# Performance work log

Hardware: AMD Instinct MI355X
Metric: run time of the kernel (lower is better)

## Reference

```python
import jax, jax.numpy as jnp
import numpy as np

D = 6          # stalk dimension
F = 64         # MLP_hidden / feature dim
N = 100_000    # num nodes
E = 20_000     # num hyperedges
NNZ = 1_000_000  # incidences
LN_EPS = 1e-5


def setup_inputs() -> dict:
    key = jax.random.key(0)
    ks = jax.random.split(key, 6)
    x = jax.random.normal(ks[0], (N * D, F), dtype=jnp.float32)
    e = jax.random.normal(ks[1], (E * D, F), dtype=jnp.float32)
    row = jax.random.randint(ks[2], (NNZ,), 0, N)   # node index per incidence
    col = jax.random.randint(ks[3], (NNZ,), 0, E)   # hyperedge index per incidence
    ln_gamma = jnp.ones((2 * F,), jnp.float32)
    ln_beta = jnp.zeros((2 * F,), jnp.float32)
    W = jax.random.normal(ks[4], (2 * F, D), dtype=jnp.float32) / np.sqrt(2 * F)
    b = jnp.zeros((D,), jnp.float32)
    return dict(x=x, e=e, row=row, col=col, ln_gamma=ln_gamma, ln_beta=ln_beta, W=W, b=b)


def reference(x, e, row, col, ln_gamma, ln_beta, W, b):
    # collapse stalk dim: [N*d, F] -> [N, F]
    n = x.shape[0] // D
    m = e.shape[0] // D
    xm = x.reshape(n, D, -1).mean(axis=1)
    em = e.reshape(m, D, -1).mean(axis=1)
    # var1 hyperedge features: gather per incidence
    xs = xm[row]            # [nnz, F]
    es = em[col]            # [nnz, F]
    h = jnp.concatenate([xs, es], axis=-1)  # [nnz, 2F]
    # sheaf_lin = input LayerNorm + Linear (num_layers=1 MLP)
    mu = h.mean(axis=-1, keepdims=True)
    var = h.var(axis=-1, keepdims=True)
    h = (h - mu) * jax.lax.rsqrt(var + LN_EPS) * ln_gamma + ln_beta
    h = h @ W + b           # [nnz, D]
    return jax.nn.sigmoid(h)  # sheaf_act='sigmoid'
```

## Files before the change

### kernel.cpp

```cpp
#include <hip/hip_runtime.h>

#define DD 6
#define FF 64
#define LN_EPS 1e-5f

template <int CTRL>
__device__ inline float dpp_mov(float x) {
    return __int_as_float(__builtin_amdgcn_update_dpp(
        0, __float_as_int(x), CTRL, 0xF, 0xF, true));
}

__global__ __launch_bounds__(256) void entity_kernel(
    const float* __restrict__ x, const float* __restrict__ e,
    const float* __restrict__ gamma, const float* __restrict__ beta,
    const float* __restrict__ W, const float* __restrict__ b,
    float* __restrict__ nodeT, float* __restrict__ edgeT,
    float* __restrict__ gwbw, int N, int E) {
    if (blockIdx.x == 0 && threadIdx.x < 12) {
        const int t = threadIdx.x;
        const int j = (t < 6) ? t : t - 6;
        const float* g = (t < 6) ? gamma : beta;
        float s = (t < 6) ? 0.f : b[j];
        for (int k = 0; k < 2 * FF; ++k) s = fmaf(g[k], W[k * DD + j], s);
        gwbw[t] = s;
    }

    const int gl = threadIdx.x & 15;
    const int nodePairs = (N + 1) >> 1;
    const int edgePairs = (E + 1) >> 1;
    const int p = blockIdx.x * 16 + (threadIdx.x >> 4);
    if (p >= nodePairs + edgePairs) return;

    const float* in; float* tab; int A, last, kbase;
    if (p < nodePairs) {
        in = x; tab = nodeT; A = 2 * p; last = N - 1; kbase = 0;
    } else {
        in = e; tab = edgeT; A = 2 * (p - nodePairs); last = E - 1; kbase = FF;
    }
    const int B = A + 1;
    const bool bval = (B <= last);
    const int Bc = bval ? B : A;

    const float4* pa = reinterpret_cast<const float4*>(in + (size_t)A * (DD * FF)) + gl;
    const float4* pb = reinterpret_cast<const float4*>(in + (size_t)Bc * (DD * FF)) + gl;
    float4 va[DD], vb[DD];
#pragma unroll
    for (int d = 0; d < DD; ++d) { va[d] = pa[d * 16]; vb[d] = pb[d * 16]; }

    float gwl[4][6];
#pragma unroll
    for (int c = 0; c < 4; ++c) {
        const int k = kbase + 4 * gl + c;
        const float g = gamma[k];
#pragma unroll
        for (int j = 0; j < 6; ++j) gwl[c][j] = g * W[k * DD + j];
    }

    float mA[4], mB[4];
    {
        float s0 = 0.f, s1 = 0.f, s2 = 0.f, s3 = 0.f;
        float u0 = 0.f, u1 = 0.f, u2 = 0.f, u3 = 0.f;
#pragma unroll
        for (int d = 0; d < DD; ++d) {
            s0 += va[d].x; s1 += va[d].y; s2 += va[d].z; s3 += va[d].w;
            u0 += vb[d].x; u1 += vb[d].y; u2 += vb[d].z; u3 += vb[d].w;
        }
        const float inv6 = 1.0f / 6.0f;
        mA[0] = s0 * inv6; mA[1] = s1 * inv6; mA[2] = s2 * inv6; mA[3] = s3 * inv6;
        mB[0] = u0 * inv6; mB[1] = u1 * inv6; mB[2] = u2 * inv6; mB[3] = u3 * inv6;
    }

    float v[16];
#pragma unroll
    for (int k = 0; k < 16; ++k) v[k] = 0.f;
#pragma unroll
    for (int c = 0; c < 4; ++c) {
        v[0] += mA[c];
        v[1] = fmaf(mA[c], mA[c], v[1]);
        v[8] += mB[c];
        v[9] = fmaf(mB[c], mB[c], v[9]);
#pragma unroll
        for (int j = 0; j < 6; ++j) {
            v[2 + j]  = fmaf(mA[c], gwl[c][j], v[2 + j]);
            v[10 + j] = fmaf(mB[c], gwl[c][j], v[10 + j]);
        }
    }

    float t[16];
#pragma unroll
    for (int k = 0; k < 16; ++k) t[k] = dpp_mov<0x140>(v[k]);
    if (gl & 8) {
#pragma unroll
        for (int k = 0; k < 8; ++k) { v[k] = v[8 + k]; t[k] = t[8 + k]; }
    }
#pragma unroll
    for (int k = 0; k < 8; ++k) v[k] += t[k];
#pragma unroll
    for (int k = 0; k < 8; ++k) t[k] = dpp_mov<0x141>(v[k]);
    if (gl & 4) {
#pragma unroll
        for (int k = 0; k < 4; ++k) { v[k] = v[4 + k]; t[k] = t[4 + k]; }
    }
#pragma unroll
    for (int k = 0; k < 4; ++k) v[k] += t[k];
#pragma unroll
    for (int k = 0; k < 4; ++k) t[k] = dpp_mov<0x4E>(v[k]);
    if (gl & 2) { v[0] = v[2]; t[0] = t[2]; v[1] = v[3]; t[1] = t[3]; }
    v[0] += t[0]; v[1] += t[1];
    t[0] = dpp_mov<0xB1>(v[0]);
    t[1] = dpp_mov<0xB1>(v[1]);
    if (gl & 1) { v[0] = v[1]; t[0] = t[1]; }
    const float r = v[0] + t[0];

    if (gl < 8) {
        tab[(size_t)A * 8 + gl] = r;
    } else if (bval) {
        tab[(size_t)B * 8 + (gl & 7)] = r;
    }
}

__global__ __launch_bounds__(256) void incidence_kernel(
    const float* __restrict__ nodeT, const float* __restrict__ edgeT,
    const int* __restrict__ row, const int* __restrict__ col,
    const float* __restrict__ gwbw, float* __restrict__ out, int nnz) {
    __shared__ float lds[4][64 * DD];
    const int wid = threadIdx.x >> 6;
    const int l = threadIdx.x & 63;
    const int i = blockIdx.x * blockDim.x + threadIdx.x;
    const int ic = min(i, nnz - 1);
    const int rr = row[ic];
    const int cc = col[ic];
    const float4* np = reinterpret_cast<const float4*>(nodeT + (size_t)rr * 8);
    const float4* ep = reinterpret_cast<const float4*>(edgeT + (size_t)cc * 8);
    const float4 a0 = np[0], a1 = np[1];
    const float4 b0 = ep[0], b1 = ep[1];

    const float S  = a0.x + b0.x;
    const float SS = a0.y + b0.y;
    const float d[6] = {a0.z + b0.z, a0.w + b0.w, a1.x + b1.x,
                        a1.y + b1.y, a1.z + b1.z, a1.w + b1.w};

    const float mu  = S * (1.0f / 128.0f);
    const float var = fmaf(SS, 1.0f / 128.0f, -mu * mu);
    const float inv = rsqrtf(var + LN_EPS);

#pragma unroll
    for (int j = 0; j < 6; ++j) {
        const float pre = fmaf(inv, fmaf(-mu, gwbw[j], d[j]), gwbw[6 + j]);
        lds[wid][l * DD + j] = 1.0f / (1.0f + __expf(-pre));
    }
    __syncthreads();
    const size_t base = (size_t)(blockIdx.x * blockDim.x + wid * 64) * DD;
    const size_t lim = (size_t)nnz * DD;
#pragma unroll
    for (int j = 0; j < 6; ++j) {
        const int f = j * 64 + l;
        if (base + (size_t)f < lim)
            __builtin_nontemporal_store(lds[wid][f], &out[base + (size_t)f]);
    }
}

extern "C" void kernel_launch(void* const* d_in, const int* in_sizes, int n_in,
                              void* d_out, int out_size, void* d_ws, size_t ws_size,
                              hipStream_t stream) {
    const float* x     = (const float*)d_in[0];
    const float* e     = (const float*)d_in[1];
    const int*   row   = (const int*)d_in[2];
    const int*   col   = (const int*)d_in[3];
    const float* gamma = (const float*)d_in[4];
    const float* beta  = (const float*)d_in[5];
    const float* W     = (const float*)d_in[6];
    const float* b     = (const float*)d_in[7];
    float* out = (float*)d_out;

    const int N   = in_sizes[0] / (DD * FF);
    const int E   = in_sizes[1] / (DD * FF);
    const int NNZ = in_sizes[2];

    float* nodeT = (float*)d_ws;
    float* edgeT = nodeT + (size_t)N * 8;
    float* gwbw  = edgeT + (size_t)E * 8;

    {
        const int totalPairs = ((N + 1) >> 1) + ((E + 1) >> 1);
        const int blocks = (totalPairs + 15) / 16;
        entity_kernel<<<blocks, 256, 0, stream>>>(x, e, gamma, beta, W, b,
                                                  nodeT, edgeT, gwbw, N, E);
    }
    {
        const int blocks = (NNZ + 255) / 256;
        incidence_kernel<<<blocks, 256, 0, stream>>>(nodeT, edgeT, row, col,
                                                     gwbw, out, NNZ);
    }
}
```

Baseline: 52.44 us.

## Fuse entity and incidence kernels into persistent kernel with grid barrier

Merges the two launches into one persistent kernel of 1024 blocks. The blocks grid-stride over node/edge pairs, meet at an atomic-counter grid barrier, then grid-stride over incidences. This removes a kernel launch and the gap between kernels. In exchange it adds a memset launch, barrier spin overhead, and the risk of deadlock if all blocks are not co-resident. The change also hoists the gamma*W loads out of the pair loop and vectorizes the output stores to float2.

```diff
diff --git a/kernel.cpp b/kernel.cpp
--- a/kernel.cpp
+++ b/kernel.cpp
@@ -3,6 +3,9 @@
 #define DD 6
 #define FF 64
 #define LN_EPS 1e-5f
+#define GRID_BLOCKS 1024
+
+typedef float f32x2 __attribute__((ext_vector_type(2)));
 
 template <int CTRL>
 __device__ inline float dpp_mov(float x) {
@@ -10,153 +13,180 @@
         0, __float_as_int(x), CTRL, 0xF, 0xF, true));
 }
 
-__global__ __launch_bounds__(256) void entity_kernel(
+__device__ inline void grid_barrier(unsigned* cnt) {
+    __syncthreads();
+    if (threadIdx.x == 0) {
+        __hip_atomic_fetch_add(cnt, 1u, __ATOMIC_ACQ_REL,
+                               __HIP_MEMORY_SCOPE_AGENT);
+        while (__hip_atomic_load(cnt, __ATOMIC_RELAXED,
+                                 __HIP_MEMORY_SCOPE_AGENT) < (unsigned)GRID_BLOCKS) {
+            __builtin_amdgcn_s_sleep(2);
+        }
+    }
+    __syncthreads();
+    __builtin_amdgcn_fence(__ATOMIC_ACQUIRE, "agent");
+}
+
+__global__ __launch_bounds__(256, 4) void fused_kernel(
     const float* __restrict__ x, const float* __restrict__ e,
     const float* __restrict__ gamma, const float* __restrict__ beta,
     const float* __restrict__ W, const float* __restrict__ b,
+    const int* __restrict__ row, const int* __restrict__ col,
     float* __restrict__ nodeT, float* __restrict__ edgeT,
-    float* __restrict__ gwbw, int N, int E) {
-    if (blockIdx.x == 0 && threadIdx.x < 12) {
-        const int t = threadIdx.x;
-        const int j = (t < 6) ? t : t - 6;
-        const float* g = (t < 6) ? gamma : beta;
-        float s = (t < 6) ? 0.f : b[j];
+    float* __restrict__ gwbw, unsigned* __restrict__ barrier_cnt,
+    float* __restrict__ out, int N, int E, int nnz) {
+    const int tid = threadIdx.x;
+
+    if (blockIdx.x == 0 && tid < 12) {
+        const int j = (tid < 6) ? tid : tid - 6;
+        const float* g = (tid < 6) ? gamma : beta;
+        float s = (tid < 6) ? 0.f : b[j];
         for (int k = 0; k < 2 * FF; ++k) s = fmaf(g[k], W[k * DD + j], s);
-        gwbw[t] = s;
+        gwbw[tid] = s;
     }
 
-    const int gl = threadIdx.x & 15;
-    const int nodePairs = (N + 1) >> 1;
-    const int edgePairs = (E + 1) >> 1;
-    const int p = blockIdx.x * 16 + (threadIdx.x >> 4);
-    if (p >= nodePairs + edgePairs) return;
-
-    const float* in; float* tab; int A, last, kbase;
-    if (p < nodePairs) {
-        in = x; tab = nodeT; A = 2 * p; last = N - 1; kbase = 0;
-    } else {
-        in = e; tab = edgeT; A = 2 * (p - nodePairs); last = E - 1; kbase = FF;
-    }
-    const int B = A + 1;
-    const bool bval = (B <= last);
-    const int Bc = bval ? B : A;
-
-    const float4* pa = reinterpret_cast<const float4*>(in + (size_t)A * (DD * FF)) + gl;
-    const float4* pb = reinterpret_cast<const float4*>(in + (size_t)Bc * (DD * FF)) + gl;
-    float4 va[DD], vb[DD];
-#pragma unroll
-    for (int d = 0; d < DD; ++d) { va[d] = pa[d * 16]; vb[d] = pb[d * 16]; }
-
-    float gwl[4][6];
-#pragma unroll
-    for (int c = 0; c < 4; ++c) {
-        const int k = kbase + 4 * gl + c;
-        const float g = gamma[k];
-#pragma unroll
-        for (int j = 0; j < 6; ++j) gwl[c][j] = g * W[k * DD + j];
-    }
-
-    float mA[4], mB[4];
-    {
-        float s0 = 0.f, s1 = 0.f, s2 = 0.f, s3 = 0.f;
-        float u0 = 0.f, u1 = 0.f, u2 = 0.f, u3 = 0.f;
-#pragma unroll
-        for (int d = 0; d < DD; ++d) {
-            s0 += va[d].x; s1 += va[d].y; s2 += va[d].z; s3 += va[d].w;
-            u0 += vb[d].x; u1 += vb[d].y; u2 += vb[d].z; u3 += vb[d].w;
-        }
-        const float inv6 = 1.0f / 6.0f;
-        mA[0] = s0 * inv6; mA[1] = s1 * inv6; mA[2] = s2 * inv6; mA[3] = s3 * inv6;
-        mB[0] = u0 * inv6; mB[1] = u1 * inv6; mB[2] = u2 * inv6; mB[3] = u3 * inv6;
-    }
-
-    float v[16];
-#pragma unroll
-    for (int k = 0; k < 16; ++k) v[k] = 0.f;
-#pragma unroll
-    for (int c = 0; c < 4; ++c) {
-        v[0] += mA[c];
-        v[1] = fmaf(mA[c], mA[c], v[1]);
-        v[8] += mB[c];
-        v[9] = fmaf(mB[c], mB[c], v[9]);
-#pragma unroll
-        for (int j = 0; j < 6; ++j) {
-            v[2 + j]  = fmaf(mA[c], gwl[c][j], v[2 + j]);
-            v[10 + j] = fmaf(mB[c], gwl[c][j], v[10 + j]);
-        }
-    }
-
-    float t[16];
-#pragma unroll
-    for (int k = 0; k < 16; ++k) t[k] = dpp_mov<0x140>(v[k]);
-    if (gl & 8) {
-#pragma unroll
-        for (int k = 0; k < 8; ++k) { v[k] = v[8 + k]; t[k] = t[8 + k]; }
-    }
-#pragma unroll
-    for (int k = 0; k < 8; ++k) v[k] += t[k];
-#pragma unroll
-    for (int k = 0; k < 8; ++k) t[k] = dpp_mov<0x141>(v[k]);
-    if (gl & 4) {
-#pragma unroll
-        for (int k = 0; k < 4; ++k) { v[k] = v[4 + k]; t[k] = t[4 + k]; }
-    }
-#pragma unroll
-    for (int k = 0; k < 4; ++k) v[k] += t[k];
-#pragma unroll
-    for (int k = 0; k < 4; ++k) t[k] = dpp_mov<0x4E>(v[k]);
-    if (gl & 2) { v[0] = v[2]; t[0] = t[2]; v[1] = v[3]; t[1] = t[3]; }
-    v[0] += t[0]; v[1] += t[1];
-    t[0] = dpp_mov<0xB1>(v[0]);
-    t[1] = dpp_mov<0xB1>(v[1]);
-    if (gl & 1) { v[0] = v[1]; t[0] = t[1]; }
-    const float r = v[0] + t[0];
-
-    if (gl < 8) {
-        tab[(size_t)A * 8 + gl] = r;
-    } else if (bval) {
-        tab[(size_t)B * 8 + (gl & 7)] = r;
-    }
-}
-
-__global__ __launch_bounds__(256) void incidence_kernel(
-    const float* __restrict__ nodeT, const float* __restrict__ edgeT,
-    const int* __restrict__ row, const int* __restrict__ col,
-    const float* __restrict__ gwbw, float* __restrict__ out, int nnz) {
+    const int gl = tid & 15;
+    const int G = gridDim.x * (blockDim.x >> 4);
+    const int g0 = blockIdx.x * (blockDim.x >> 4) + (tid >> 4);
+
+    auto section = [&](const float* __restrict__ in, float* __restrict__ tab,
+                       int kbase, int cnt) {
+        const int pairs = (cnt + 1) >> 1;
+        float gwl[4][6];
+#pragma unroll
+        for (int c = 0; c < 4; ++c) {
+            const int k = kbase + 4 * gl + c;
+            const float gk = gamma[k];
+#pragma unroll
+            for (int j = 0; j < 6; ++j) gwl[c][j] = gk * W[k * DD + j];
+        }
+        for (int p = g0; p < pairs; p += G) {
+            const int A = 2 * p;
+            const bool bval = (A + 1 < cnt);
+            const int Bc = bval ? A + 1 : A;
+            const float4* pa =
+                reinterpret_cast<const float4*>(in + (size_t)A * (DD * FF)) + gl;
+            const float4* pb =
+                reinterpret_cast<const float4*>(in + (size_t)Bc * (DD * FF)) + gl;
+            float4 sA = pa[0];
+            float4 sB = pb[0];
+#pragma unroll
+            for (int d = 1; d < DD; ++d) {
+                const float4 ta = pa[d * 16], tb = pb[d * 16];
+                sA.x += ta.x; sA.y += ta.y; sA.z += ta.z; sA.w += ta.w;
+                sB.x += tb.x; sB.y += tb.y; sB.z += tb.z; sB.w += tb.w;
+            }
+            const float inv6 = 1.0f / 6.0f;
+            const float mA[4] = {sA.x * inv6, sA.y * inv6, sA.z * inv6, sA.w * inv6};
+            const float mB[4] = {sB.x * inv6, sB.y * inv6, sB.z * inv6, sB.w * inv6};
+
+            float v[16];
+#pragma unroll
+            for (int k = 0; k < 16; ++k) v[k] = 0.f;
+#pragma unroll
+            for (int c = 0; c < 4; ++c) {
+                v[0] += mA[c];
+                v[1] = fmaf(mA[c], mA[c], v[1]);
+                v[8] += mB[c];
+                v[9] = fmaf(mB[c], mB[c], v[9]);
+#pragma unroll
+                for (int j = 0; j < 6; ++j) {
+                    v[2 + j]  = fmaf(mA[c], gwl[c][j], v[2 + j]);
+                    v[10 + j] = fmaf(mB[c], gwl[c][j], v[10 + j]);
+                }
+            }
+            float t[16];
+#pragma unroll
+            for (int k = 0; k < 16; ++k) t[k] = dpp_mov<0x140>(v[k]);
+            if (gl & 8) {
+#pragma unroll
+                for (int k = 0; k < 8; ++k) { v[k] = v[8 + k]; t[k] = t[8 + k]; }
+            }
+#pragma unroll
+            for (int k = 0; k < 8; ++k) v[k] += t[k];
+#pragma unroll
+            for (int k = 0; k < 8; ++k) t[k] = dpp_mov<0x141>(v[k]);
+            if (gl & 4) {
+#pragma unroll
+                for (int k = 0; k < 4; ++k) { v[k] = v[4 + k]; t[k] = t[4 + k]; }
+            }
+#pragma unroll
+            for (int k = 0; k < 4; ++k) v[k] += t[k];
+#pragma unroll
+            for (int k = 0; k < 4; ++k) t[k] = dpp_mov<0x4E>(v[k]);
+            if (gl & 2) { v[0] = v[2]; t[0] = t[2]; v[1] = v[3]; t[1] = t[3]; }
+            v[0] += t[0]; v[1] += t[1];
+            t[0] = dpp_mov<0xB1>(v[0]);
+            t[1] = dpp_mov<0xB1>(v[1]);
+            if (gl & 1) { v[0] = v[1]; t[0] = t[1]; }
+            const float r = v[0] + t[0];
+
+            if (gl < 8) {
+                tab[(size_t)A * 8 + gl] = r;
+            } else if (bval) {
+                tab[(size_t)(A + 1) * 8 + (gl & 7)] = r;
+            }
+        }
+    };
+    section(x, nodeT, 0, N);
+    section(e, edgeT, FF, E);
+
+    grid_barrier(barrier_cnt);
+
+    float gwv[12];
+#pragma unroll
+    for (int j = 0; j < 12; ++j) gwv[j] = gwbw[j];
+
     __shared__ float lds[4][64 * DD];
-    const int wid = threadIdx.x >> 6;
-    const int l = threadIdx.x & 63;
-    const int i = blockIdx.x * blockDim.x + threadIdx.x;
-    const int ic = min(i, nnz - 1);
-    const int rr = row[ic];
-    const int cc = col[ic];
-    const float4* np = reinterpret_cast<const float4*>(nodeT + (size_t)rr * 8);
-    const float4* ep = reinterpret_cast<const float4*>(edgeT + (size_t)cc * 8);
-    const float4 a0 = np[0], a1 = np[1];
-    const float4 b0 = ep[0], b1 = ep[1];
-
-    const float S  = a0.x + b0.x;
-    const float SS = a0.y + b0.y;
-    const float d[6] = {a0.z + b0.z, a0.w + b0.w, a1.x + b1.x,
-                        a1.y + b1.y, a1.z + b1.z, a1.w + b1.w};
-
-    const float mu  = S * (1.0f / 128.0f);
-    const float var = fmaf(SS, 1.0f / 128.0f, -mu * mu);
-    const float inv = rsqrtf(var + LN_EPS);
-
-#pragma unroll
-    for (int j = 0; j < 6; ++j) {
-        const float pre = fmaf(inv, fmaf(-mu, gwbw[j], d[j]), gwbw[6 + j]);
-        lds[wid][l * DD + j] = 1.0f / (1.0f + __expf(-pre));
-    }
-    __syncthreads();
-    const size_t base = (size_t)(blockIdx.x * blockDim.x + wid * 64) * DD;
+    const int wid = tid >> 6;
+    const int l = tid & 63;
     const size_t lim = (size_t)nnz * DD;
-#pragma unroll
-    for (int j = 0; j < 6; ++j) {
-        const int f = j * 64 + l;
-        if (base + (size_t)f < lim)
-            __builtin_nontemporal_store(lds[wid][f], &out[base + (size_t)f]);
+    const int nblk = (nnz + 63) >> 6;
+
+    for (int sb = blockIdx.x; sb * 4 < nblk; sb += gridDim.x) {
+        const int bb = sb * 4 + wid;
+        const bool active = (bb < nblk);
+        if (active) {
+            const int i = bb * 64 + l;
+            const int ic = min(i, nnz - 1);
+            const int rr = row[ic];
+            const int cc = col[ic];
+            const float4* np =
+                reinterpret_cast<const float4*>(nodeT + (size_t)rr * 8);
+            const float4* ep =
+                reinterpret_cast<const float4*>(edgeT + (size_t)cc * 8);
+            const float4 a0 = np[0], a1 = np[1];
+            const float4 e0 = ep[0], e1 = ep[1];
+
+            const float S  = a0.x + e0.x;
+            const float SS = a0.y + e0.y;
+            const float d[6] = {a0.z + e0.z, a0.w + e0.w, a1.x + e1.x,
+                                a1.y + e1.y, a1.z + e1.z, a1.w + e1.w};
+
+            const float mu  = S * (1.0f / 128.0f);
+            const float var = fmaf(SS, 1.0f / 128.0f, -mu * mu);
+            const float inv = rsqrtf(var + LN_EPS);
+
+#pragma unroll
+            for (int j = 0; j < 6; ++j) {
+                const float pre = fmaf(inv, fmaf(-mu, gwv[j], d[j]), gwv[6 + j]);
+                lds[wid][l * DD + j] = 1.0f / (1.0f + __expf(-pre));
+            }
+        }
+        __syncthreads();
+        if (active) {
+            const size_t base = (size_t)bb * (64 * DD);
+#pragma unroll
+            for (int j2 = 0; j2 < 3; ++j2) {
+                const int f = j2 * 128 + 2 * l;
+                if (base + (size_t)f < lim) {
+                    const f32x2 v2 = *reinterpret_cast<const f32x2*>(&lds[wid][f]);
+                    __builtin_nontemporal_store(
+                        v2, reinterpret_cast<f32x2*>(&out[base + (size_t)f]));
+                }
+            }
+        }
+        __syncthreads();
     }
 }
 
@@ -173,23 +203,18 @@
     const float* b     = (const float*)d_in[7];
     float* out = (float*)d_out;
 
-    const int N   = in_sizes[0] / (DD * FF);
-    const int E   = in_sizes[1] / (DD * FF);
-    const int NNZ = in_sizes[2];
+    int N   = in_sizes[0] / (DD * FF);
+    int E   = in_sizes[1] / (DD * FF);
+    int NNZ = in_sizes[2];
 
     float* nodeT = (float*)d_ws;
     float* edgeT = nodeT + (size_t)N * 8;
     float* gwbw  = edgeT + (size_t)E * 8;
-
-    {
-        const int totalPairs = ((N + 1) >> 1) + ((E + 1) >> 1);
-        const int blocks = (totalPairs + 15) / 16;
-        entity_kernel<<<blocks, 256, 0, stream>>>(x, e, gamma, beta, W, b,
-                                                  nodeT, edgeT, gwbw, N, E);
-    }
-    {
-        const int blocks = (NNZ + 255) / 256;
-        incidence_kernel<<<blocks, 256, 0, stream>>>(nodeT, edgeT, row, col,
-                                                     gwbw, out, NNZ);
-    }
-}
+    unsigned* barrier_cnt = (unsigned*)(gwbw + 20);
+
+    (void)hipMemsetAsync((void*)barrier_cnt, 0, sizeof(unsigned), stream);
+
+    fused_kernel<<<GRID_BLOCKS, 256, 0, stream>>>(
+        x, e, gamma, beta, W, b, row, col,
+        nodeT, edgeT, gwbw, barrier_cnt, out, N, E, NNZ);
+}
```

Measured after the change: 185.0 us. +252.8%, slower.
